# Optimization experiments

Hardware: AMD Instinct MI355X
Metric: run time of the kernel (lower is better)

The kernel has to match this reference:

```python
import jax, jax.numpy as jnp
import numpy as np

EMBED = 512
HEADS = 8
HEAD_DIM = EMBED // HEADS


def setup_inputs() -> dict:
    key = jax.random.key(0)
    ks = jax.random.split(key, 12)
    B, L, D = 2, 4096, EMBED
    s = 1.0 / np.sqrt(D)  # torch Linear default init range scale (approx, uniform)
    def lin(k):
        kw, kb = jax.random.split(k)
        W = jax.random.uniform(kw, (D, D), jnp.float32, -s, s)
        b = jax.random.uniform(kb, (D,), jnp.float32, -s, s)
        return W, b
    Wq, bq = lin(ks[0])
    Wk, bk = lin(ks[1])
    Wv, bv = lin(ks[2])
    Wo, bo = lin(ks[3])
    query = jax.random.normal(ks[4], (B, L, D), jnp.float32)
    key_t = jax.random.normal(ks[5], (B, L, D), jnp.float32)
    value = jax.random.normal(ks[6], (B, L, D), jnp.float32)
    return {"query": query, "key": key_t, "value": value,
            "Wq": Wq, "bq": bq, "Wk": Wk, "bk": bk,
            "Wv": Wv, "bv": bv, "Wo": Wo, "bo": bo}


def reference(query, key, value, Wq, bq, Wk, bk, Wv, bv, Wo, bo):
    B, L, D = query.shape
    H, Hd = HEADS, HEAD_DIM
    scale = Hd ** -0.5
    # torch nn.Linear: y = x @ W.T + b
    q = (query @ Wq.T + bq).reshape(B, L, H, Hd).transpose(0, 2, 1, 3)   # [B,H,L,Hd]
    k = (key   @ Wk.T + bk).reshape(B, -1, H, Hd).transpose(0, 2, 1, 3)
    v = (value @ Wv.T + bv).reshape(B, -1, H, Hd).transpose(0, 2, 1, 3)
    scores = jnp.einsum('bhqd,bhkd->bhqk', q, k) * scale                  # [B,H,L,L]
    causal = jnp.triu(jnp.ones((L, L), dtype=bool), k=1)                  # True above diag
    neg = jnp.finfo(scores.dtype).min
    scores = jnp.where(causal, neg, scores)
    attn = jax.nn.softmax(scores, axis=-1)
    # dropout is identity in eval mode
    out = jnp.einsum('bhqk,bhkd->bhqd', attn, v)                          # [B,H,L,Hd]
    out = out.transpose(0, 2, 1, 3).reshape(B, L, D)
    return out @ Wo.T + bo, attn
```

## Files before the change

kernel.cpp:

```cpp
#include <hip/hip_runtime.h>
#include <hip/hip_bf16.h>


typedef __attribute__((ext_vector_type(8))) __bf16 bf16x8;
typedef __attribute__((ext_vector_type(4))) __bf16 bf16v4;
typedef __attribute__((ext_vector_type(4))) float f32x4;

constexpr int LL = 4096;
constexpr int DD = 512;
constexpr int HH = 8;
constexpr int HD = 64;
constexpr int BB = 2;
constexpr int BL = BB * LL;
constexpr size_t OUT_ELEMS = (size_t)BB * LL * DD;
constexpr int CH = 8;
constexpr int NCHUNK = LL / 64 / CH;
constexpr int CHUNKS_PER_BH = 288;

static __device__ inline int chunk_off(int qb) {
    const int g = qb >> 3, r = qb & 7;
    return qb + 4 * g * (g - 1) + r * g;
}

static __device__ inline bf16x8 cvt8(const float* p) {
    float4 a = *reinterpret_cast<const float4*>(p);
    float4 b = *reinterpret_cast<const float4*>(p + 4);
    bf16x8 r;
    r[0] = (__bf16)a.x; r[1] = (__bf16)a.y; r[2] = (__bf16)a.z; r[3] = (__bf16)a.w;
    r[4] = (__bf16)b.x; r[5] = (__bf16)b.y; r[6] = (__bf16)b.z; r[7] = (__bf16)b.w;
    return r;
}

__global__ __launch_bounds__(256) void cvt_kernel(
    const float* __restrict__ q, const float* __restrict__ k,
    const float* __restrict__ v, __bf16* __restrict__ o)
{
    constexpr size_t N = (size_t)BL * DD;
    size_t i = ((size_t)blockIdx.x * 256 + threadIdx.x) * 8;
    const float* src = q; size_t j = i;
    if (i >= 2 * N)      { src = v; j = i - 2 * N; }
    else if (i >= N)     { src = k; j = i - N; }
    *reinterpret_cast<bf16x8*>(&o[i]) = cvt8(&src[j]);
}

__global__ __launch_bounds__(256) void zero_kernel(float* __restrict__ attn_out)
{
    const int bh = blockIdx.x;
    const int qb = blockIdx.y;
    const int z  = blockIdx.z;

    const int wv   = threadIdx.x >> 6;
    const int lane = threadIdx.x & 63;

    const int strip = 1024 - (qb + 1) * 16;
    const int col0  = (qb + 1) * 64 + z * strip;
    float* base = attn_out + (size_t)bh * LL * LL + (size_t)qb * 64 * LL;

    const f32x4 z4 = {0.f, 0.f, 0.f, 0.f};
    for (int r = wv; r < 64; r += 4) {
        float* row = base + (size_t)r * LL + col0;
        for (int c = lane * 4; c < strip; c += 256)
            *reinterpret_cast<f32x4*>(row + c) = z4;
    }
}

__global__ __launch_bounds__(256) void qkv_kernel(
    const __bf16* __restrict__ Xb,
    const float* __restrict__ Wq, const float* __restrict__ bq,
    const float* __restrict__ Wk, const float* __restrict__ bk,
    const float* __restrict__ Wv, const float* __restrict__ bv,
    __bf16* __restrict__ Qb, __bf16* __restrict__ Kb, __bf16* __restrict__ Vt)
{
    const int z = blockIdx.z;
    const __bf16* x  = Xb + (size_t)z * BL * DD;
    const float* W   = (z == 0) ? Wq : (z == 1) ? Wk : Wv;
    const float* bia = (z == 0) ? bq : (z == 1) ? bk : bv;

    const int wid = threadIdx.x >> 6;
    const int lane = threadIdx.x & 63;
    const int l15 = lane & 15;
    const int lg  = lane >> 4;

    const int r0 = blockIdx.x * 64;
    const int cb = blockIdx.y;
    const int c0 = cb * 64 + wid * 16;

    f32x4 acc[4] = {};
    for (int k0 = 0; k0 < DD; k0 += 32) {
        bf16x8 bfrag = cvt8(&W[(size_t)(c0 + l15) * DD + k0 + lg * 8]);
#pragma unroll
        for (int mt = 0; mt < 4; ++mt) {
            bf16x8 afrag = *reinterpret_cast<const bf16x8*>(
                &x[(size_t)(r0 + mt * 16 + l15) * DD + k0 + lg * 8]);
            acc[mt] = __builtin_amdgcn_mfma_f32_16x16x32_bf16(afrag, bfrag, acc[mt], 0, 0, 0);
        }
    }

    __shared__ __bf16 T[64][72];
    const float bval = bia[c0 + l15];
#pragma unroll
    for (int mt = 0; mt < 4; ++mt)
#pragma unroll
        for (int i = 0; i < 4; ++i) {
            const float val = acc[mt][i] + bval;
            const int row = mt * 16 + lg * 4 + i;
            const int col = wid * 16 + l15;
            if (z == 2) T[col][row] = (__bf16)val;
            else        T[row][col] = (__bf16)val;
        }
    __syncthreads();

    const int tr  = threadIdx.x >> 2;
    const int seg = threadIdx.x & 3;
    uint4 v0 = *reinterpret_cast<const uint4*>(&T[tr][seg * 16]);
    uint4 v1 = *reinterpret_cast<const uint4*>(&T[tr][seg * 16 + 8]);
    const int b  = r0 >> 12;
    const int l0 = r0 & (LL - 1);
    if (z == 2) {
        __bf16* dst = Vt + ((size_t)(b * HH + cb) * HD + tr) * LL + l0 + seg * 16;
        *reinterpret_cast<uint4*>(dst)     = v0;
        *reinterpret_cast<uint4*>(dst + 8) = v1;
    } else {
        __bf16* base = (z == 0) ? Qb : Kb;
        __bf16* dst = base + ((size_t)(b * HH + cb) * LL + l0 + tr) * HD + seg * 16;
        *reinterpret_cast<uint4*>(dst)     = v0;
        *reinterpret_cast<uint4*>(dst + 8) = v1;
    }
}

__global__ __launch_bounds__(256, 4) void rowsum_kernel(
    const __bf16* __restrict__ Qb, const __bf16* __restrict__ Kb,
    float* __restrict__ rspart)
{
    const int bh = blockIdx.x;
    const int qb = 63 - blockIdx.y;
    const int ch = blockIdx.z;
    const int kb0 = ch * CH;
    if (kb0 > qb) return;

    const int wv   = threadIdx.x >> 6;
    const int lane = threadIdx.x & 63;
    const int l15  = lane & 15;
    const int lg   = lane >> 4;

    const __bf16* Qh = Qb + (size_t)bh * LL * HD;
    const __bf16* Kh = Kb + (size_t)bh * LL * HD;

    const int q0 = qb * 64 + wv * 16;
    const int qrow = q0 + l15;
    const bf16x8 qf0 = *reinterpret_cast<const bf16x8*>(&Qh[(size_t)qrow * HD + lg * 8]);
    const bf16x8 qf1 = *reinterpret_cast<const bf16x8*>(&Qh[(size_t)qrow * HD + 32 + lg * 8]);
    const float SC = 0.125f * 1.44269504088896f;

    auto loadK = [&](bf16x8 (&kf)[8], int kb) {
        const __bf16* kp = &Kh[((size_t)kb * 64 + l15) * HD + lg * 8];
#pragma unroll
        for (int kt = 0; kt < 4; ++kt) {
            kf[kt * 2]     = *reinterpret_cast<const bf16x8*>(kp + (size_t)kt * 16 * HD);
            kf[kt * 2 + 1] = *reinterpret_cast<const bf16x8*>(kp + (size_t)kt * 16 * HD + 32);
        }
    };

    float rs = 0.f;
    auto body = [&](bf16x8 (&kf)[8], int kb) {
        f32x4 s[4] = {};
#pragma unroll
        for (int kt = 0; kt < 4; ++kt) {
            s[kt] = __builtin_amdgcn_mfma_f32_16x16x32_bf16(kf[kt * 2],     qf0, s[kt], 0, 0, 0);
            s[kt] = __builtin_amdgcn_mfma_f32_16x16x32_bf16(kf[kt * 2 + 1], qf1, s[kt], 0, 0, 0);
        }
        const bool diag = (kb == qb);
#pragma unroll
        for (int kt = 0; kt < 4; ++kt)
#pragma unroll
            for (int i = 0; i < 4; ++i) {
                float e = exp2f(s[kt][i] * SC);
                if (diag && (kb * 64 + kt * 16 + lg * 4 + i) > qrow) e = 0.f;
                rs += e;
            }
    };

    const int kend = (qb < kb0 + CH - 1) ? qb : kb0 + CH - 1;
    {
        bf16x8 kA[8], kB[8];
        int kb = kb0;
        bool useA = true;
        loadK(kA, kb);
        for (; kb <= kend; ++kb) {
            if (useA) { if (kb + 1 <= kend) loadK(kB, kb + 1); body(kA, kb); }
            else      { if (kb + 1 <= kend) loadK(kA, kb + 1); body(kB, kb); }
            useA = !useA;
        }
    }
    rs += __shfl_xor(rs, 16, 64);
    rs += __shfl_xor(rs, 32, 64);
    if (lane < 16)
        rspart[((size_t)bh * LL + qrow) * NCHUNK + ch] = rs;
}

__global__ __launch_bounds__(256, 3) void attn_main_kernel(
    const __bf16* __restrict__ Qb, const __bf16* __restrict__ Kb,
    const __bf16* __restrict__ Vt, const float* __restrict__ rspart,
    __bf16* __restrict__ opart, float* __restrict__ attn_out)
{
    const int bh = blockIdx.x;
    const int qb = 63 - blockIdx.y;
    const int ch = blockIdx.z;
    const int kb0 = ch * CH;
    if (kb0 > qb) return;

    const int wv   = threadIdx.x >> 6;
    const int lane = threadIdx.x & 63;
    const int l15  = lane & 15;
    const int lg   = lane >> 4;

    float* A_out = attn_out + (size_t)bh * LL * LL;
    const int q0 = qb * 64 + wv * 16;
    const int qrow = q0 + l15;

    const __bf16* Qh = Qb + (size_t)bh * LL * HD;
    const __bf16* Kh = Kb + (size_t)bh * LL * HD;
    const __bf16* Vh = Vt + (size_t)bh * HD * LL;

    __shared__ float  Pf[4][16][68];
    __shared__ __bf16 Pb[4][16][72];

    const bf16x8 qf0 = *reinterpret_cast<const bf16x8*>(&Qh[(size_t)qrow * HD + lg * 8]);
    const bf16x8 qf1 = *reinterpret_cast<const bf16x8*>(&Qh[(size_t)qrow * HD + 32 + lg * 8]);

    float rsv = 0.f;
    const int nc = qb >> 3;
    const float* rp = &rspart[((size_t)bh * LL + qrow) * NCHUNK];
    for (int c = 0; c <= nc; ++c) rsv += rp[c];
    const float llog = -log2f(rsv);
    const float SC = 0.125f * 1.44269504088896f;

    f32x4 oacc[4] = {};

    const int srow = lane >> 4;
    const int scol = (lane & 15) * 4;

    auto loadK = [&](bf16x8 (&kf)[8], int kb) {
        const __bf16* kp = &Kh[((size_t)kb * 64 + l15) * HD + lg * 8];
#pragma unroll
        for (int kt = 0; kt < 4; ++kt) {
            kf[kt * 2]     = *reinterpret_cast<const bf16x8*>(kp + (size_t)kt * 16 * HD);
            kf[kt * 2 + 1] = *reinterpret_cast<const bf16x8*>(kp + (size_t)kt * 16 * HD + 32);
        }
    };

    auto body = [&](bf16x8 (&kf)[8], int kb) {
        bf16x8 vf[8];
        {
            const __bf16* vp = &Vh[(size_t)l15 * LL + (size_t)kb * 64 + lg * 8];
#pragma unroll
            for (int ht = 0; ht < 4; ++ht) {
                vf[ht * 2]     = *reinterpret_cast<const bf16x8*>(vp + (size_t)ht * 16 * LL);
                vf[ht * 2 + 1] = *reinterpret_cast<const bf16x8*>(vp + (size_t)ht * 16 * LL + 32);
            }
        }
        f32x4 s[4] = {};
#pragma unroll
        for (int kt = 0; kt < 4; ++kt) {
            s[kt] = __builtin_amdgcn_mfma_f32_16x16x32_bf16(kf[kt * 2],     qf0, s[kt], 0, 0, 0);
            s[kt] = __builtin_amdgcn_mfma_f32_16x16x32_bf16(kf[kt * 2 + 1], qf1, s[kt], 0, 0, 0);
        }
        const bool diag = (kb == qb);
#pragma unroll
        for (int kt = 0; kt < 4; ++kt) {
            float e0 = exp2f(fmaf(s[kt][0], SC, llog));
            float e1 = exp2f(fmaf(s[kt][1], SC, llog));
            float e2 = exp2f(fmaf(s[kt][2], SC, llog));
            float e3 = exp2f(fmaf(s[kt][3], SC, llog));
            if (diag) {
                const int kc = kb * 64 + kt * 16 + lg * 4;
                if (kc + 0 > qrow) e0 = 0.f;
                if (kc + 1 > qrow) e1 = 0.f;
                if (kc + 2 > qrow) e2 = 0.f;
                if (kc + 3 > qrow) e3 = 0.f;
            }
            f32x4 ev = {e0, e1, e2, e3};
            *reinterpret_cast<f32x4*>(&Pf[wv][l15][kt * 16 + lg * 4]) = ev;
            bf16v4 pk;
            pk[0] = (__bf16)e0; pk[1] = (__bf16)e1;
            pk[2] = (__bf16)e2; pk[3] = (__bf16)e3;
            *reinterpret_cast<bf16v4*>(&Pb[wv][l15][kt * 16 + lg * 4]) = pk;
        }
#pragma unroll
        for (int rq = 0; rq < 4; ++rq) {
            const int row = rq * 4 + srow;
            f32x4 v = *reinterpret_cast<const f32x4*>(&Pf[wv][row][scol]);
            *reinterpret_cast<f32x4*>(
                &A_out[(size_t)(q0 + row) * LL + kb * 64 + scol]) = v;
        }
        const bf16x8 pa0 = *reinterpret_cast<const bf16x8*>(&Pb[wv][l15][lg * 8]);
        const bf16x8 pa1 = *reinterpret_cast<const bf16x8*>(&Pb[wv][l15][32 + lg * 8]);
#pragma unroll
        for (int ht = 0; ht < 4; ++ht) {
            oacc[ht] = __builtin_amdgcn_mfma_f32_16x16x32_bf16(pa0, vf[ht * 2],     oacc[ht], 0, 0, 0);
            oacc[ht] = __builtin_amdgcn_mfma_f32_16x16x32_bf16(pa1, vf[ht * 2 + 1], oacc[ht], 0, 0, 0);
        }
    };

    const int kend = (qb < kb0 + CH - 1) ? qb : kb0 + CH - 1;
    {
        bf16x8 kA[8], kB[8];
        int kb = kb0;
        bool useA = true;
        loadK(kA, kb);
        for (; kb <= kend; ++kb) {
            if (useA) { if (kb + 1 <= kend) loadK(kB, kb + 1); body(kA, kb); }
            else      { if (kb + 1 <= kend) loadK(kA, kb + 1); body(kB, kb); }
            useA = !useA;
        }
    }

#pragma unroll
    for (int ht = 0; ht < 4; ++ht)
#pragma unroll
        for (int i = 0; i < 4; ++i)
            Pb[wv][lg * 4 + i][ht * 16 + l15] = (__bf16)oacc[ht][i];
    const int arow = lane >> 2;
    const int aseg = lane & 3;
    uint4 o0 = *reinterpret_cast<const uint4*>(&Pb[wv][arow][aseg * 16]);
    uint4 o1 = *reinterpret_cast<const uint4*>(&Pb[wv][arow][aseg * 16 + 8]);
    __bf16* dst = opart
        + ((size_t)(bh * CHUNKS_PER_BH + chunk_off(qb) + ch)) * 4096
        + (wv * 16 + arow) * 64 + aseg * 16;
    *reinterpret_cast<uint4*>(dst)     = o0;
    *reinterpret_cast<uint4*>(dst + 8) = o1;
}

__global__ __launch_bounds__(256) void oreduce_kernel(
    const __bf16* __restrict__ opart, __bf16* __restrict__ Ob)
{
    const int bh = blockIdx.x;
    const int qb = blockIdx.y;
    const int nc = qb >> 3;
    const __bf16* src = opart + ((size_t)(bh * CHUNKS_PER_BH + chunk_off(qb))) * 4096;
    const int t = threadIdx.x;

    float acc[16] = {};
    for (int c = 0; c <= nc; ++c) {
        bf16x8 a = *reinterpret_cast<const bf16x8*>(&src[(size_t)c * 4096 + t * 16]);
        bf16x8 b = *reinterpret_cast<const bf16x8*>(&src[(size_t)c * 4096 + t * 16 + 8]);
#pragma unroll
        for (int j = 0; j < 8; ++j) { acc[j] += (float)a[j]; acc[8 + j] += (float)b[j]; }
    }
    bf16x8 r0, r1;
#pragma unroll
    for (int j = 0; j < 8; ++j) { r0[j] = (__bf16)acc[j]; r1[j] = (__bf16)acc[8 + j]; }

    const int qr  = t >> 2;
    const int hd0 = (t & 3) * 16;
    const int b = bh >> 3, h = bh & 7;
    __bf16* dst = Ob + ((size_t)(b * LL + qb * 64 + qr)) * DD + h * HD + hd0;
    *reinterpret_cast<bf16x8*>(dst)     = r0;
    *reinterpret_cast<bf16x8*>(dst + 8) = r1;
}

__global__ __launch_bounds__(256) void oproj_kernel(
    const __bf16* __restrict__ Ob, const float* __restrict__ Wo,
    const float* __restrict__ bo, float* __restrict__ out)
{
    const int wid = threadIdx.x >> 6;
    const int lane = threadIdx.x & 63;
    const int l15 = lane & 15;
    const int lg  = lane >> 4;

    const int r0 = blockIdx.x * 64;
    const int c0 = blockIdx.y * 64 + wid * 16;

    f32x4 acc[4] = {};
    for (int k0 = 0; k0 < DD; k0 += 32) {
        bf16x8 bfrag = cvt8(&Wo[(size_t)(c0 + l15) * DD + k0 + lg * 8]);
#pragma unroll
        for (int mt = 0; mt < 4; ++mt) {
            bf16x8 afrag = *reinterpret_cast<const bf16x8*>(
                &Ob[(size_t)(r0 + mt * 16 + l15) * DD + k0 + lg * 8]);
            acc[mt] = __builtin_amdgcn_mfma_f32_16x16x32_bf16(afrag, bfrag, acc[mt], 0, 0, 0);
        }
    }
    const float bval = bo[c0 + l15];
#pragma unroll
    for (int mt = 0; mt < 4; ++mt)
#pragma unroll
        for (int i = 0; i < 4; ++i)
            out[(size_t)(r0 + mt * 16 + lg * 4 + i) * DD + c0 + l15] = acc[mt][i] + bval;
}

extern "C" void kernel_launch(void* const* d_in, const int* in_sizes, int n_in,
                              void* d_out, int out_size, void* d_ws, size_t ws_size,
                              hipStream_t stream) {
    const float* query = (const float*)d_in[0];
    const float* key_t = (const float*)d_in[1];
    const float* value = (const float*)d_in[2];
    const float* Wq = (const float*)d_in[3];
    const float* bq = (const float*)d_in[4];
    const float* Wk = (const float*)d_in[5];
    const float* bk = (const float*)d_in[6];
    const float* Wv = (const float*)d_in[7];
    const float* bv = (const float*)d_in[8];
    const float* Wo = (const float*)d_in[9];
    const float* bo = (const float*)d_in[10];

    float* out  = (float*)d_out;
    float* attn = out + OUT_ELEMS;

    char* ws = (char*)d_ws;
    __bf16* Qb     = (__bf16*)(ws);
    __bf16* Kb     = (__bf16*)(ws +  8388608);
    __bf16* Vt     = (__bf16*)(ws + 16777216);
    __bf16* Ob     = (__bf16*)(ws + 25165824);
    float*  rspart = (float*) (ws + 33554432);
    __bf16* Xb     = (__bf16*)(ws + 35651584);
    __bf16* opart  = (__bf16*)(ws + 35651584);

    cvt_kernel<<<dim3(3 * BL * DD / 8 / 256), 256, 0, stream>>>(query, key_t, value, Xb);
    zero_kernel<<<dim3(BB * HH, LL / 64 - 1, 4), 256, 0, stream>>>(attn);
    qkv_kernel<<<dim3(BL / 64, DD / 64, 3), 256, 0, stream>>>(
        Xb, Wq, bq, Wk, bk, Wv, bv, Qb, Kb, Vt);
    rowsum_kernel<<<dim3(BB * HH, LL / 64, NCHUNK), 256, 0, stream>>>(Qb, Kb, rspart);
    attn_main_kernel<<<dim3(BB * HH, LL / 64, NCHUNK), 256, 0, stream>>>(
        Qb, Kb, Vt, rspart, opart, attn);
    oreduce_kernel<<<dim3(BB * HH, LL / 64), 256, 0, stream>>>(opart, Ob);
    oproj_kernel<<<dim3(BL / 64, DD / 64), 256, 0, stream>>>(Ob, Wo, bo, out);
}
```

Before: 819.6 us.

## Batch attention-prob stores via bf16 LDS staging over four key blocks

Drops the separate fp32 LDS tile for the attention probabilities and keeps only the bf16 probability tile, widened to hold four key blocks. The attention matrix is written to global in batches of 256 contiguous columns per row, rebuilding fp32 from bf16, instead of 64 columns after every key block. This aims to cut LDS traffic and footprint and to make the global stores longer and more coalesced. The returned attention values now carry bf16 precision, which changes the fp32 output accuracy.

Measured after the change: 856.4 us. 1.04x slower.

```diff
diff --git a/kernel.cpp b/kernel.cpp
--- a/kernel.cpp
+++ b/kernel.cpp
@@ -5,6 +5,7 @@
 typedef __attribute__((ext_vector_type(8))) __bf16 bf16x8;
 typedef __attribute__((ext_vector_type(4))) __bf16 bf16v4;
 typedef __attribute__((ext_vector_type(4))) float f32x4;
+typedef __attribute__((ext_vector_type(4))) unsigned short u16x4;
 
 constexpr int LL = 4096;
 constexpr int DD = 512;
@@ -222,8 +223,7 @@
     const __bf16* Kh = Kb + (size_t)bh * LL * HD;
     const __bf16* Vh = Vt + (size_t)bh * HD * LL;
 
-    __shared__ float  Pf[4][16][68];
-    __shared__ __bf16 Pb[4][16][72];
+    __shared__ __bf16 Pbuf[4][16][264];
 
     const bf16x8 qf0 = *reinterpret_cast<const bf16x8*>(&Qh[(size_t)qrow * HD + lg * 8]);
     const bf16x8 qf1 = *reinterpret_cast<const bf16x8*>(&Qh[(size_t)qrow * HD + 32 + lg * 8]);
@@ -237,9 +237,6 @@
 
     f32x4 oacc[4] = {};
 
-    const int srow = lane >> 4;
-    const int scol = (lane & 15) * 4;
-
     auto loadK = [&](bf16x8 (&kf)[8], int kb) {
         const __bf16* kp = &Kh[((size_t)kb * 64 + l15) * HD + lg * 8];
 #pragma unroll
@@ -249,7 +246,7 @@
         }
     };
 
-    auto body = [&](bf16x8 (&kf)[8], int kb) {
+    auto body = [&](bf16x8 (&kf)[8], int kb, int tt) {
         bf16x8 vf[8];
         {
             const __bf16* vp = &Vh[(size_t)l15 * LL + (size_t)kb * 64 + lg * 8];
@@ -279,22 +276,13 @@
                 if (kc + 2 > qrow) e2 = 0.f;
                 if (kc + 3 > qrow) e3 = 0.f;
             }
-            f32x4 ev = {e0, e1, e2, e3};
-            *reinterpret_cast<f32x4*>(&Pf[wv][l15][kt * 16 + lg * 4]) = ev;
             bf16v4 pk;
             pk[0] = (__bf16)e0; pk[1] = (__bf16)e1;
             pk[2] = (__bf16)e2; pk[3] = (__bf16)e3;
-            *reinterpret_cast<bf16v4*>(&Pb[wv][l15][kt * 16 + lg * 4]) = pk;
-        }
-#pragma unroll
-        for (int rq = 0; rq < 4; ++rq) {
-            const int row = rq * 4 + srow;
-            f32x4 v = *reinterpret_cast<const f32x4*>(&Pf[wv][row][scol]);
-            *reinterpret_cast<f32x4*>(
-                &A_out[(size_t)(q0 + row) * LL + kb * 64 + scol]) = v;
-        }
-        const bf16x8 pa0 = *reinterpret_cast<const bf16x8*>(&Pb[wv][l15][lg * 8]);
-        const bf16x8 pa1 = *reinterpret_cast<const bf16x8*>(&Pb[wv][l15][32 + lg * 8]);
+            *reinterpret_cast<bf16v4*>(&Pbuf[wv][l15][tt * 64 + kt * 16 + lg * 4]) = pk;
+        }
+        const bf16x8 pa0 = *reinterpret_cast<const bf16x8*>(&Pbuf[wv][l15][tt * 64 + lg * 8]);
+        const bf16x8 pa1 = *reinterpret_cast<const bf16x8*>(&Pbuf[wv][l15][tt * 64 + 32 + lg * 8]);
 #pragma unroll
         for (int ht = 0; ht < 4; ++ht) {
             oacc[ht] = __builtin_amdgcn_mfma_f32_16x16x32_bf16(pa0, vf[ht * 2],     oacc[ht], 0, 0, 0);
@@ -302,16 +290,38 @@
         }
     };
 
+    auto flush = [&](int mp, int vt) {
+        if (lane * 4 < vt * 64) {
+            const int colbase = kb0 * 64 + mp * 256 + lane * 4;
+#pragma unroll
+            for (int r = 0; r < 16; ++r) {
+                u16x4 u = *reinterpret_cast<const u16x4*>(&Pbuf[wv][r][lane * 4]);
+                f32x4 v;
+                v[0] = __uint_as_float((unsigned)u[0] << 16);
+                v[1] = __uint_as_float((unsigned)u[1] << 16);
+                v[2] = __uint_as_float((unsigned)u[2] << 16);
+                v[3] = __uint_as_float((unsigned)u[3] << 16);
+                *reinterpret_cast<f32x4*>(&A_out[(size_t)(q0 + r) * LL + colbase]) = v;
+            }
+        }
+    };
+
     const int kend = (qb < kb0 + CH - 1) ? qb : kb0 + CH - 1;
+    const int nv = kend - kb0 + 1;
     {
         bf16x8 kA[8], kB[8];
         int kb = kb0;
         bool useA = true;
         loadK(kA, kb);
-        for (; kb <= kend; ++kb) {
-            if (useA) { if (kb + 1 <= kend) loadK(kB, kb + 1); body(kA, kb); }
-            else      { if (kb + 1 <= kend) loadK(kA, kb + 1); body(kB, kb); }
-            useA = !useA;
+        for (int mp = 0; mp < 2; ++mp) {
+            const int vt = (nv - mp * 4 < 4) ? nv - mp * 4 : 4;
+            if (vt <= 0) break;
+            for (int tt = 0; tt < vt; ++tt, ++kb) {
+                if (useA) { if (kb + 1 <= kend) loadK(kB, kb + 1); body(kA, kb, tt); }
+                else      { if (kb + 1 <= kend) loadK(kA, kb + 1); body(kB, kb, tt); }
+                useA = !useA;
+            }
+            flush(mp, vt);
         }
     }
 
@@ -319,11 +329,11 @@
     for (int ht = 0; ht < 4; ++ht)
 #pragma unroll
         for (int i = 0; i < 4; ++i)
-            Pb[wv][lg * 4 + i][ht * 16 + l15] = (__bf16)oacc[ht][i];
+            Pbuf[wv][lg * 4 + i][ht * 16 + l15] = (__bf16)oacc[ht][i];
     const int arow = lane >> 2;
     const int aseg = lane & 3;
-    uint4 o0 = *reinterpret_cast<const uint4*>(&Pb[wv][arow][aseg * 16]);
-    uint4 o1 = *reinterpret_cast<const uint4*>(&Pb[wv][arow][aseg * 16 + 8]);
+    uint4 o0 = *reinterpret_cast<const uint4*>(&Pbuf[wv][arow][aseg * 16]);
+    uint4 o1 = *reinterpret_cast<const uint4*>(&Pbuf[wv][arow][aseg * 16 + 8]);
     __bf16* dst = opart
         + ((size_t)(bh * CHUNKS_PER_BH + chunk_off(qb) + ch)) * 4096
         + (wv * 16 + arow) * 64 + aseg * 16;
```
